# Kernel optimization log

Hardware: AMD Instinct MI355X
Metric: run time of the kernel (lower is better)

## Reference

```python
import jax, jax.numpy as jnp
import numpy as np

D_MODEL = 2048
N_EXPERTS = 64


def setup_inputs() -> dict:
    key = jax.random.key(0)
    kx, kw = jax.random.split(key)
    x = jax.random.normal(kx, (4, 4096, D_MODEL), dtype=jnp.float32)
    # nn.Linear(d_model, n_experts, bias=False): weight [n_experts, d_model]
    W = jax.random.normal(kw, (N_EXPERTS, D_MODEL), dtype=jnp.float32) * (1.0 / np.sqrt(D_MODEL))
    return {"x": x, "W": W, "n_active": 2, "capacity": 4096}


def reference(x, W, n_active, capacity):
    # router_logits = x @ W^T : [b, s, e]
    router_logits = jnp.einsum("bsd,ed->bse", x, W)
    router_probs = jax.nn.softmax(router_logits, axis=-1)
    # top-k over experts
    scores, expert_indices = jax.lax.top_k(router_probs, n_active)  # [b, s, k]
    scores = scores / jnp.sum(scores, axis=-1, keepdims=True)
    n_experts = router_probs.shape[-1]
    # scatter normalized scores into dense gate tensor [b, s, e]
    # (top-k indices are distinct, so one-hot sum == torch scatter_)
    gates = jnp.sum(
        jax.nn.one_hot(expert_indices, n_experts, dtype=scores.dtype) * scores[..., None],
        axis=-2,
    )
    expert_counts = jnp.sum(gates, axis=(0, 1))  # [e]
    load_loss = jnp.mean((expert_counts / jnp.sum(expert_counts) * n_experts - 1.0) ** 2)
    return gates, expert_indices, load_loss
```

## Files before the change

kernel.cpp:

```cpp
#include <hip/hip_runtime.h>
#include <hip/hip_bf16.h>
#include <math.h>

#define TOK_TOTAL 16384
#define D_MODEL   2048
#define NEXP      64
#define KQ        1024
#define NCHQ      (KQ / 32)
#define TAU       1e-3f

#define IDX_OFF   (TOK_TOTAL * NEXP)
#define LOSS_OFF  (IDX_OFF + TOK_TOTAL * 2)

#define WS_WH     (TOK_TOTAL * NEXP)
#define WS_WL     (WS_WH + 65536)
#define WS_CNTP   (WS_WL + 65536)
#define WS_RCNT   (WS_CNTP + 16384)
#define WS_RLIST  (WS_RCNT + 1)

typedef __attribute__((ext_vector_type(8))) short short8_t;
typedef __attribute__((ext_vector_type(4))) float f32x4;

__device__ inline void cvt_hl(float4 a, float4 b, short8_t& h8, short8_t& l8)
{
    const float f[8] = {a.x, a.y, a.z, a.w, b.x, b.y, b.z, b.w};
    #pragma unroll
    for (int j = 0; j < 8; ++j) {
        __hip_bfloat16 h = __float2bfloat16(f[j]);
        h8[j] = __builtin_bit_cast(short, h);
        l8[j] = __builtin_bit_cast(short, __float2bfloat16(f[j] - __bfloat162float(h)));
    }
}

__global__ __launch_bounds__(256, 1)
void build_wt(const float* __restrict__ W, short8_t* __restrict__ WH8,
              short8_t* __restrict__ WL8, int* __restrict__ rep_cnt)
{
    const int id = blockIdx.x * 256 + threadIdx.x;
    if (id == 0) *rep_cnt = 0;
    const int k8 = id & 255, e = id >> 8;
    float4 a = *(const float4*)(W + (long)e * D_MODEL + k8 * 8);
    float4 b = *(const float4*)(W + (long)e * D_MODEL + k8 * 8 + 4);
    short8_t h8, l8;
    cvt_hl(a, b, h8, l8);
    WH8[k8 * NEXP + e] = h8;
    WL8[k8 * NEXP + e] = l8;
}

__global__ __launch_bounds__(256, 2)
void router_gemm(const float* __restrict__ x,
                 const short8_t* __restrict__ WH8, const short8_t* __restrict__ WL8,
                 float* __restrict__ p0, float* __restrict__ p1)
{
    const int t = threadIdx.x;
    const int w = t >> 6, l = t & 63;
    const int kh = blockIdx.x & 1;
    const long tokw = (long)(blockIdx.x >> 1) * 64 + w * 16;
    const int lane16 = l & 15, kq = l >> 4;
    const long kb0 = (long)kh * KQ;

    const float* xp = x + (tokw + lane16) * D_MODEL + kb0 + kq * 8;
    const short8_t* whp = WH8 + (kb0 / 8 + kq) * NEXP + lane16;
    const short8_t* wlp = WL8 + (kb0 / 8 + kq) * NEXP + lane16;

    f32x4 acc[4];
    #pragma unroll
    for (int nt = 0; nt < 4; ++nt) acc[nt] = (f32x4){0.f, 0.f, 0.f, 0.f};

    float4 xa = *(const float4*)(xp);
    float4 xb = *(const float4*)(xp + 4);

    #pragma unroll 2
    for (int ic = 0; ic < NCHQ; ++ic) {
        short8_t ah, al;
        cvt_hl(xa, xb, ah, al);
        if (ic + 1 < NCHQ) {
            xa = *(const float4*)(xp + 32 * (ic + 1));
            xb = *(const float4*)(xp + 32 * (ic + 1) + 4);
        }
        const short8_t* wh = whp + (long)ic * 4 * NEXP;
        const short8_t* wl = wlp + (long)ic * 4 * NEXP;
        #pragma unroll
        for (int nt = 0; nt < 4; ++nt) {
            short8_t bh = wh[nt * 16];
            short8_t bl = wl[nt * 16];
            acc[nt] = __builtin_amdgcn_mfma_f32_16x16x32_bf16(ah, bl, acc[nt], 0, 0, 0);
            acc[nt] = __builtin_amdgcn_mfma_f32_16x16x32_bf16(al, bh, acc[nt], 0, 0, 0);
            acc[nt] = __builtin_amdgcn_mfma_f32_16x16x32_bf16(ah, bh, acc[nt], 0, 0, 0);
        }
    }

    float* dst = kh ? p1 : p0;
    #pragma unroll
    for (int nt = 0; nt < 4; ++nt)
        #pragma unroll
        for (int r = 0; r < 4; ++r)
            dst[(tokw + kq * 4 + r) * NEXP + nt * 16 + lane16] = acc[nt][r];
}

__global__ __launch_bounds__(256, 1)
void router_combine(const float* __restrict__ p0, const float* __restrict__ p1,
                    float* __restrict__ out, float* __restrict__ cntp,
                    int* __restrict__ rep_cnt, int* __restrict__ rep_list)
{
    __shared__ float4 s_ig[64];
    const int t = threadIdx.x;
    const int r = t >> 2, q = t & 3;
    const long tok0 = (long)blockIdx.x * 64;
    const long tok  = tok0 + r;

    float v[16];
    {
        const float4* a4 = (const float4*)(p0 + tok * NEXP) + q * 4;
        const float4* b4 = (const float4*)(p1 + tok * NEXP) + q * 4;
        #pragma unroll
        for (int j = 0; j < 4; ++j) {
            float4 a = a4[j], b = b4[j];
            v[j*4+0] = a.x + b.x; v[j*4+1] = a.y + b.y;
            v[j*4+2] = a.z + b.z; v[j*4+3] = a.w + b.w;
        }
    }

    float b0 = -1e30f, b1 = -1e30f, b2 = -1e30f;
    int i0 = 0, i1 = 0;
    const int ebase = q * 16;
    #pragma unroll
    for (int j = 0; j < 16; ++j) {
        float xv = v[j]; int e = ebase + j;
        if (xv > b0)      { b2 = b1; b1 = b0; i1 = i0; b0 = xv; i0 = e; }
        else if (xv > b1) { b2 = b1; b1 = xv; i1 = e; }
        else if (xv > b2) { b2 = xv; }
    }

    #pragma unroll
    for (int d = 1; d <= 2; d <<= 1) {
        float ob0 = __shfl_xor(b0, d, 64), ob1 = __shfl_xor(b1, d, 64), ob2 = __shfl_xor(b2, d, 64);
        int   oi0 = __shfl_xor(i0, d, 64), oi1 = __shfl_xor(i1, d, 64);
        bool a0w = (b0 > ob0) || (b0 == ob0 && i0 < oi0);
        float nb0 = a0w ? b0 : ob0;  int ni0 = a0w ? i0 : oi0;
        float ca  = a0w ? b1 : ob1;  int cia = a0w ? i1 : oi1;
        float cb  = a0w ? ob0 : b0;  int cib = a0w ? oi0 : i0;
        float wa2 = a0w ? b2 : ob2;
        float lb1 = a0w ? ob1 : b1;
        bool w1 = (ca > cb) || (ca == cb && cia < cib);
        float nb1 = w1 ? ca : cb;  int ni1 = w1 ? cia : cib;
        float nb2 = w1 ? fmaxf(wa2, cb) : fmaxf(ca, lb1);
        b0 = nb0; i0 = ni0; b1 = nb1; i1 = ni1; b2 = nb2;
    }

    float ex = __expf(b1 - b0);
    float g0 = 1.f / (1.f + ex);
    float g1 = ex * g0;

    {
        float* orow = out + tok * NEXP + ebase;
        #pragma unroll
        for (int j4 = 0; j4 < 4; ++j4) {
            float gv[4];
            #pragma unroll
            for (int j = 0; j < 4; ++j) {
                int e = ebase + j4 * 4 + j;
                gv[j] = (e == i0) ? g0 : ((e == i1) ? g1 : 0.f);
            }
            *(float4*)(orow + j4 * 4) = make_float4(gv[0], gv[1], gv[2], gv[3]);
        }
    }

    if (q == 0) {
        out[IDX_OFF + 2 * tok]     = (float)i0;
        out[IDX_OFF + 2 * tok + 1] = (float)i1;
        s_ig[r] = make_float4((float)i0, (float)i1, g0, g1);
        if ((b0 - b1 < TAU) || (b1 - b2 < TAU)) {
            int p = atomicAdd(rep_cnt, 1);
            rep_list[p] = (int)tok;
        }
    }
    __syncthreads();

    if (t < 64) {
        float c = 0.f;
        for (int tt = 0; tt < 64; ++tt) {
            float4 gg = s_ig[tt];
            if ((int)gg.x == t) c += gg.z;
            if ((int)gg.y == t) c += gg.w;
        }
        cntp[blockIdx.x * NEXP + t] = c;
    }
}

__global__ __launch_bounds__(256, 1)
void router_tail(const float* __restrict__ x, const float* __restrict__ W,
                 float* __restrict__ out, const float* __restrict__ cntp,
                 const int* __restrict__ rep_cnt, const int* __restrict__ rep_list)
{
    const int t = threadIdx.x;

    if (blockIdx.x == 0) {
        __shared__ double red[4][NEXP];
        const int e = t & 63, p = t >> 6;
        double s = 0.0;
        for (int b = 0; b < 64; ++b)
            s += (double)cntp[(p * 64 + b) * NEXP + e];
        red[p][e] = s;
        __syncthreads();
        if (t == 0) {
            double sc[NEXP], tot = 0.0;
            for (int i = 0; i < NEXP; ++i) {
                sc[i] = red[0][i] + red[1][i] + red[2][i] + red[3][i];
                tot += sc[i];
            }
            double loss = 0.0;
            for (int i = 0; i < NEXP; ++i) {
                double d = sc[i] / tot * (double)NEXP - 1.0;
                loss += d * d;
            }
            out[LOSS_OFF] = (float)(loss / NEXP);
        }
        return;
    }

    __shared__ double red[4][NEXP];
    const int nf = *rep_cnt;
    const int e = t & 63, part = t >> 6;
    for (int i = (int)blockIdx.x - 1; i < nf; i += (int)gridDim.x - 1) {
        const long tok = rep_list[i];
        const float* xr = x + tok * D_MODEL;
        const float* wr = W + (long)e * D_MODEL;
        const int k0 = part * 512;
        double s = 0.0;
        for (int kk = 0; kk < 512; kk += 4) {
            float4 xv = *(const float4*)(xr + k0 + kk);
            float4 wv = *(const float4*)(wr + k0 + kk);
            s = fma((double)xv.x, (double)wv.x, s);
            s = fma((double)xv.y, (double)wv.y, s);
            s = fma((double)xv.z, (double)wv.z, s);
            s = fma((double)xv.w, (double)wv.w, s);
        }
        red[part][e] = s;
        __syncthreads();
        if (t == 0) {
            double best = -1e300, sec = -1e300;
            int bi = 0, si = 0;
            for (int ee = 0; ee < NEXP; ++ee) {
                double vv = red[0][ee] + red[1][ee] + red[2][ee] + red[3][ee];
                if (vv > best)     { sec = best; si = bi; best = vv; bi = ee; }
                else if (vv > sec) { sec = vv; si = ee; }
            }
            out[IDX_OFF + 2 * tok]     = (float)bi;
            out[IDX_OFF + 2 * tok + 1] = (float)si;
        }
        __syncthreads();
    }
}

extern "C" void kernel_launch(void* const* d_in, const int* in_sizes, int n_in,
                              void* d_out, int out_size, void* d_ws, size_t ws_size,
                              hipStream_t stream)
{
    const float* x = (const float*)d_in[0];
    const float* W = (const float*)d_in[1];
    float* out = (float*)d_out;
    float* ws  = (float*)d_ws;
    float* p0  = out;
    float* p1  = ws;
    short8_t* WH8 = (short8_t*)(ws + WS_WH);
    short8_t* WL8 = (short8_t*)(ws + WS_WL);
    float* cntp = ws + WS_CNTP;
    int* rep_cnt  = (int*)(ws + WS_RCNT);
    int* rep_list = (int*)(ws + WS_RLIST);

    build_wt      <<<64, 256, 0, stream>>>(W, WH8, WL8, rep_cnt);
    router_gemm   <<<(TOK_TOTAL / 64) * 2, 256, 0, stream>>>(x, WH8, WL8, p0, p1);
    router_combine<<<TOK_TOTAL / 64, 256, 0, stream>>>(p0, p1, out, cntp, rep_cnt, rep_list);
    router_tail   <<<257, 256, 0, stream>>>(x, W, out, cntp, rep_cnt, rep_list);
}
```

Before: 83.73 us.

## Fuse router GEMM with top-k epilogue using LDS-staged split-bf16 x tiles

Replaces the split-K GEMM plus separate combine kernel with one kernel. Each block handles 32 tokens over the full K dimension. x chunks are converted once to hi/lo bf16 and double-buffered in shared memory, and four waves share that A tile across two expert halves. Top-k, gates, indices, the near-tie list and per-block counts are computed in the epilogue from logits held in LDS. This removes the partial-logit round trip through global memory and one kernel launch. The cost is block-level synchronisation, a serial 64-expert top-k scan in 32 threads, and twice as many count partials for the tail to reduce.

```diff
diff --git a/kernel.cpp b/kernel.cpp
--- a/kernel.cpp
+++ b/kernel.cpp
@@ -5,31 +5,30 @@
 #define TOK_TOTAL 16384
 #define D_MODEL   2048
 #define NEXP      64
-#define KQ        1024
-#define NCHQ      (KQ / 32)
+#define BM        32
+#define KC        256
+#define NCH       (D_MODEL / KC)
+#define PADS      264
+#define NBLK      (TOK_TOTAL / BM)
 #define TAU       1e-3f
 
 #define IDX_OFF   (TOK_TOTAL * NEXP)
 #define LOSS_OFF  (IDX_OFF + TOK_TOTAL * 2)
 
-#define WS_WH     (TOK_TOTAL * NEXP)
-#define WS_WL     (WS_WH + 65536)
-#define WS_CNTP   (WS_WL + 65536)
-#define WS_RCNT   (WS_CNTP + 16384)
+#define WS_WL     65536
+#define WS_CNTP   (2 * 65536)
+#define WS_RCNT   (WS_CNTP + NBLK * NEXP)
 #define WS_RLIST  (WS_RCNT + 1)
 
 typedef __attribute__((ext_vector_type(8))) short short8_t;
 typedef __attribute__((ext_vector_type(4))) float f32x4;
 
-__device__ inline void cvt_hl(float4 a, float4 b, short8_t& h8, short8_t& l8)
-{
-    const float f[8] = {a.x, a.y, a.z, a.w, b.x, b.y, b.z, b.w};
-    #pragma unroll
-    for (int j = 0; j < 8; ++j) {
-        __hip_bfloat16 h = __float2bfloat16(f[j]);
-        h8[j] = __builtin_bit_cast(short, h);
-        l8[j] = __builtin_bit_cast(short, __float2bfloat16(f[j] - __bfloat162float(h)));
-    }
+__device__ __forceinline__ short cvh(float f) {
+    return __builtin_bit_cast(short, __float2bfloat16(f));
+}
+__device__ __forceinline__ short cvl(float f) {
+    __hip_bfloat16 h = __float2bfloat16(f);
+    return __builtin_bit_cast(short, __float2bfloat16(f - __bfloat162float(h)));
 }
 
 __global__ __launch_bounds__(256, 1)
@@ -42,7 +41,10 @@
     float4 a = *(const float4*)(W + (long)e * D_MODEL + k8 * 8);
     float4 b = *(const float4*)(W + (long)e * D_MODEL + k8 * 8 + 4);
     short8_t h8, l8;
-    cvt_hl(a, b, h8, l8);
+    h8[0]=cvh(a.x); h8[1]=cvh(a.y); h8[2]=cvh(a.z); h8[3]=cvh(a.w);
+    h8[4]=cvh(b.x); h8[5]=cvh(b.y); h8[6]=cvh(b.z); h8[7]=cvh(b.w);
+    l8[0]=cvl(a.x); l8[1]=cvl(a.y); l8[2]=cvl(a.z); l8[3]=cvl(a.w);
+    l8[4]=cvl(b.x); l8[5]=cvl(b.y); l8[6]=cvl(b.z); l8[7]=cvl(b.w);
     WH8[k8 * NEXP + e] = h8;
     WL8[k8 * NEXP + e] = l8;
 }
@@ -50,126 +52,101 @@
 __global__ __launch_bounds__(256, 2)
 void router_gemm(const float* __restrict__ x,
                  const short8_t* __restrict__ WH8, const short8_t* __restrict__ WL8,
-                 float* __restrict__ p0, float* __restrict__ p1)
-{
-    const int t = threadIdx.x;
-    const int w = t >> 6, l = t & 63;
-    const int kh = blockIdx.x & 1;
-    const long tokw = (long)(blockIdx.x >> 1) * 64 + w * 16;
+                 float* __restrict__ out, float* __restrict__ cntp,
+                 int* __restrict__ rep_cnt, int* __restrict__ rep_list)
+{
+    __shared__ __align__(16) short sx[2][2][BM][PADS];
+    __shared__ float4 s_ig[BM];
+
+    const int t  = threadIdx.x;
+    const int w  = t >> 6, l = t & 63;
+    const int tg = w >> 1, eg = w & 1;
     const int lane16 = l & 15, kq = l >> 4;
-    const long kb0 = (long)kh * KQ;
-
-    const float* xp = x + (tokw + lane16) * D_MODEL + kb0 + kq * 8;
-    const short8_t* whp = WH8 + (kb0 / 8 + kq) * NEXP + lane16;
-    const short8_t* wlp = WL8 + (kb0 / 8 + kq) * NEXP + lane16;
-
-    f32x4 acc[4];
-    #pragma unroll
-    for (int nt = 0; nt < 4; ++nt) acc[nt] = (f32x4){0.f, 0.f, 0.f, 0.f};
-
-    float4 xa = *(const float4*)(xp);
-    float4 xb = *(const float4*)(xp + 4);
-
-    #pragma unroll 2
-    for (int ic = 0; ic < NCHQ; ++ic) {
-        short8_t ah, al;
-        cvt_hl(xa, xb, ah, al);
-        if (ic + 1 < NCHQ) {
-            xa = *(const float4*)(xp + 32 * (ic + 1));
-            xb = *(const float4*)(xp + 32 * (ic + 1) + 4);
-        }
-        const short8_t* wh = whp + (long)ic * 4 * NEXP;
-        const short8_t* wl = wlp + (long)ic * 4 * NEXP;
-        #pragma unroll
-        for (int nt = 0; nt < 4; ++nt) {
-            short8_t bh = wh[nt * 16];
-            short8_t bl = wl[nt * 16];
-            acc[nt] = __builtin_amdgcn_mfma_f32_16x16x32_bf16(ah, bl, acc[nt], 0, 0, 0);
-            acc[nt] = __builtin_amdgcn_mfma_f32_16x16x32_bf16(al, bh, acc[nt], 0, 0, 0);
-            acc[nt] = __builtin_amdgcn_mfma_f32_16x16x32_bf16(ah, bh, acc[nt], 0, 0, 0);
-        }
-    }
-
-    float* dst = kh ? p1 : p0;
-    #pragma unroll
-    for (int nt = 0; nt < 4; ++nt)
-        #pragma unroll
-        for (int r = 0; r < 4; ++r)
-            dst[(tokw + kq * 4 + r) * NEXP + nt * 16 + lane16] = acc[nt][r];
-}
-
-__global__ __launch_bounds__(256, 1)
-void router_combine(const float* __restrict__ p0, const float* __restrict__ p1,
-                    float* __restrict__ out, float* __restrict__ cntp,
-                    int* __restrict__ rep_cnt, int* __restrict__ rep_list)
-{
-    __shared__ float4 s_ig[64];
-    const int t = threadIdx.x;
-    const int r = t >> 2, q = t & 3;
-    const long tok0 = (long)blockIdx.x * 64;
-    const long tok  = tok0 + r;
-
-    float v[16];
+    const long tok0 = (long)blockIdx.x * BM;
+
+    const int srow = t >> 3;
+    const int sseg = t & 7;
+
+    f32x4 acc0 = (f32x4){0.f,0.f,0.f,0.f};
+    f32x4 acc1 = (f32x4){0.f,0.f,0.f,0.f};
+
+    float4 xr[8];
+
+    auto LOADX = [&](int c) {
+        const float* g = x + (tok0 + srow) * D_MODEL + c * KC + sseg * 4;
+        #pragma unroll
+        for (int j = 0; j < 8; ++j) xr[j] = *(const float4*)(g + j * 32);
+    };
+    auto STOREX = [&](int buf) {
+        #pragma unroll
+        for (int j = 0; j < 8; ++j) {
+            short4 h, lo;
+            h.x = cvh(xr[j].x); h.y = cvh(xr[j].y); h.z = cvh(xr[j].z); h.w = cvh(xr[j].w);
+            lo.x = cvl(xr[j].x); lo.y = cvl(xr[j].y); lo.z = cvl(xr[j].z); lo.w = cvl(xr[j].w);
+            *(short4*)(&sx[buf][0][srow][sseg * 4 + j * 32]) = h;
+            *(short4*)(&sx[buf][1][srow][sseg * 4 + j * 32]) = lo;
+        }
+    };
+
+    const short8_t* whk = WH8 + (long)kq * NEXP + eg * 32 + lane16;
+    const short8_t* wlk = WL8 + (long)kq * NEXP + eg * 32 + lane16;
+    const int arow = tg * 16 + lane16;
+
+    LOADX(0);
+    STOREX(0);
+    __syncthreads();
+
+    for (int c = 0; c < NCH; ++c) {
+        const int buf = c & 1;
+        const bool pre = (c + 1 < NCH);
+        if (pre) LOADX(c + 1);
+        #pragma unroll
+        for (int g = 0; g < 8; ++g) {
+            short8_t ah = *(const short8_t*)(&sx[buf][0][arow][g * 32 + kq * 8]);
+            short8_t al = *(const short8_t*)(&sx[buf][1][arow][g * 32 + kq * 8]);
+            const long k8off = (long)(c * 32 + g * 4) * NEXP;
+            short8_t bh0 = whk[k8off];
+            short8_t bl0 = wlk[k8off];
+            short8_t bh1 = whk[k8off + 16];
+            short8_t bl1 = wlk[k8off + 16];
+            acc0 = __builtin_amdgcn_mfma_f32_16x16x32_bf16(ah, bl0, acc0, 0, 0, 0);
+            acc0 = __builtin_amdgcn_mfma_f32_16x16x32_bf16(al, bh0, acc0, 0, 0, 0);
+            acc0 = __builtin_amdgcn_mfma_f32_16x16x32_bf16(ah, bh0, acc0, 0, 0, 0);
+            acc1 = __builtin_amdgcn_mfma_f32_16x16x32_bf16(ah, bl1, acc1, 0, 0, 0);
+            acc1 = __builtin_amdgcn_mfma_f32_16x16x32_bf16(al, bh1, acc1, 0, 0, 0);
+            acc1 = __builtin_amdgcn_mfma_f32_16x16x32_bf16(ah, bh1, acc1, 0, 0, 0);
+        }
+        if (pre) STOREX(buf ^ 1);
+        __syncthreads();
+    }
+
+    float* Lg = (float*)&sx[0][0][0][0];
     {
-        const float4* a4 = (const float4*)(p0 + tok * NEXP) + q * 4;
-        const float4* b4 = (const float4*)(p1 + tok * NEXP) + q * 4;
-        #pragma unroll
-        for (int j = 0; j < 4; ++j) {
-            float4 a = a4[j], b = b4[j];
-            v[j*4+0] = a.x + b.x; v[j*4+1] = a.y + b.y;
-            v[j*4+2] = a.z + b.z; v[j*4+3] = a.w + b.w;
-        }
-    }
-
-    float b0 = -1e30f, b1 = -1e30f, b2 = -1e30f;
-    int i0 = 0, i1 = 0;
-    const int ebase = q * 16;
-    #pragma unroll
-    for (int j = 0; j < 16; ++j) {
-        float xv = v[j]; int e = ebase + j;
-        if (xv > b0)      { b2 = b1; b1 = b0; i1 = i0; b0 = xv; i0 = e; }
-        else if (xv > b1) { b2 = b1; b1 = xv; i1 = e; }
-        else if (xv > b2) { b2 = xv; }
-    }
-
-    #pragma unroll
-    for (int d = 1; d <= 2; d <<= 1) {
-        float ob0 = __shfl_xor(b0, d, 64), ob1 = __shfl_xor(b1, d, 64), ob2 = __shfl_xor(b2, d, 64);
-        int   oi0 = __shfl_xor(i0, d, 64), oi1 = __shfl_xor(i1, d, 64);
-        bool a0w = (b0 > ob0) || (b0 == ob0 && i0 < oi0);
-        float nb0 = a0w ? b0 : ob0;  int ni0 = a0w ? i0 : oi0;
-        float ca  = a0w ? b1 : ob1;  int cia = a0w ? i1 : oi1;
-        float cb  = a0w ? ob0 : b0;  int cib = a0w ? oi0 : i0;
-        float wa2 = a0w ? b2 : ob2;
-        float lb1 = a0w ? ob1 : b1;
-        bool w1 = (ca > cb) || (ca == cb && cia < cib);
-        float nb1 = w1 ? ca : cb;  int ni1 = w1 ? cia : cib;
-        float nb2 = w1 ? fmaxf(wa2, cb) : fmaxf(ca, lb1);
-        b0 = nb0; i0 = ni0; b1 = nb1; i1 = ni1; b2 = nb2;
-    }
-
-    float ex = __expf(b1 - b0);
-    float g0 = 1.f / (1.f + ex);
-    float g1 = ex * g0;
-
-    {
-        float* orow = out + tok * NEXP + ebase;
-        #pragma unroll
-        for (int j4 = 0; j4 < 4; ++j4) {
-            float gv[4];
-            #pragma unroll
-            for (int j = 0; j < 4; ++j) {
-                int e = ebase + j4 * 4 + j;
-                gv[j] = (e == i0) ? g0 : ((e == i1) ? g1 : 0.f);
-            }
-            *(float4*)(orow + j4 * 4) = make_float4(gv[0], gv[1], gv[2], gv[3]);
-        }
-    }
-
-    if (q == 0) {
+        const int trow = tg * 16 + kq * 4;
+        #pragma unroll
+        for (int r = 0; r < 4; ++r) {
+            Lg[(trow + r) * 68 + eg * 32 + lane16]      = acc0[r];
+            Lg[(trow + r) * 68 + eg * 32 + 16 + lane16] = acc1[r];
+        }
+    }
+    __syncthreads();
+
+    if (t < BM) {
+        const float* lrow = Lg + t * 68;
+        float b0 = -1e30f, b1 = -1e30f, b2 = -1e30f;
+        int i0 = 0, i1 = 0;
+        for (int e = 0; e < NEXP; ++e) {
+            float v = lrow[e];
+            if (v > b0)      { b2 = b1; b1 = b0; i1 = i0; b0 = v; i0 = e; }
+            else if (v > b1) { b2 = b1; b1 = v; i1 = e; }
+            else if (v > b2) { b2 = v; }
+        }
+        float ex = __expf(b1 - b0);
+        float g0 = 1.f / (1.f + ex);
+        long tok = tok0 + t;
         out[IDX_OFF + 2 * tok]     = (float)i0;
         out[IDX_OFF + 2 * tok + 1] = (float)i1;
-        s_ig[r] = make_float4((float)i0, (float)i1, g0, g1);
+        s_ig[t] = make_float4((float)i0, (float)i1, g0, ex * g0);
         if ((b0 - b1 < TAU) || (b1 - b2 < TAU)) {
             int p = atomicAdd(rep_cnt, 1);
             rep_list[p] = (int)tok;
@@ -177,14 +154,29 @@
     }
     __syncthreads();
 
-    if (t < 64) {
-        float c = 0.f;
-        for (int tt = 0; tt < 64; ++tt) {
+    {
+        const int r8 = t >> 3, e0 = (t & 7) * 8;
+        float4 gg = s_ig[r8];
+        const int i0 = (int)gg.x, i1 = (int)gg.y;
+        float v[8];
+        #pragma unroll
+        for (int j = 0; j < 8; ++j) {
+            int e = e0 + j;
+            v[j] = (e == i0) ? gg.z : ((e == i1) ? gg.w : 0.f);
+        }
+        float* orow = out + (tok0 + r8) * NEXP + e0;
+        *(float4*)(orow)     = make_float4(v[0], v[1], v[2], v[3]);
+        *(float4*)(orow + 4) = make_float4(v[4], v[5], v[6], v[7]);
+    }
+
+    if (t < NEXP) {
+        float cs = 0.f;
+        for (int tt = 0; tt < BM; ++tt) {
             float4 gg = s_ig[tt];
-            if ((int)gg.x == t) c += gg.z;
-            if ((int)gg.y == t) c += gg.w;
-        }
-        cntp[blockIdx.x * NEXP + t] = c;
+            if ((int)gg.x == t) cs += gg.z;
+            if ((int)gg.y == t) cs += gg.w;
+        }
+        cntp[blockIdx.x * NEXP + t] = cs;
     }
 }
 
@@ -199,8 +191,8 @@
         __shared__ double red[4][NEXP];
         const int e = t & 63, p = t >> 6;
         double s = 0.0;
-        for (int b = 0; b < 64; ++b)
-            s += (double)cntp[(p * 64 + b) * NEXP + e];
+        for (int b = 0; b < NBLK / 4; ++b)
+            s += (double)cntp[(p * (NBLK / 4) + b) * NEXP + e];
         red[p][e] = s;
         __syncthreads();
         if (t == 0) {
@@ -261,16 +253,13 @@
     const float* W = (const float*)d_in[1];
     float* out = (float*)d_out;
     float* ws  = (float*)d_ws;
-    float* p0  = out;
-    float* p1  = ws;
-    short8_t* WH8 = (short8_t*)(ws + WS_WH);
+    short8_t* WH8 = (short8_t*)ws;
     short8_t* WL8 = (short8_t*)(ws + WS_WL);
     float* cntp = ws + WS_CNTP;
     int* rep_cnt  = (int*)(ws + WS_RCNT);
     int* rep_list = (int*)(ws + WS_RLIST);
 
-    build_wt      <<<64, 256, 0, stream>>>(W, WH8, WL8, rep_cnt);
-    router_gemm   <<<(TOK_TOTAL / 64) * 2, 256, 0, stream>>>(x, WH8, WL8, p0, p1);
-    router_combine<<<TOK_TOTAL / 64, 256, 0, stream>>>(p0, p1, out, cntp, rep_cnt, rep_list);
-    router_tail   <<<257, 256, 0, stream>>>(x, W, out, cntp, rep_cnt, rep_list);
-}
+    build_wt   <<<64, 256, 0, stream>>>(W, WH8, WL8, rep_cnt);
+    router_gemm<<<NBLK, 256, 0, stream>>>(x, WH8, WL8, out, cntp, rep_cnt, rep_list);
+    router_tail<<<257, 256, 0, stream>>>(x, W, out, cntp, rep_cnt, rep_list);
+}
```

New measurement: 96.91 us. 1.16x slower.
